# Optimization experiments

Measured on AMD Instinct MI355X. Metric: run time of the kernel, lower is better.

## Reference

```python
import jax, jax.numpy as jnp
import numpy as np

N_IN = 512
N_OUT = 256
K = 3
GRID_SIZE = N_OUT - K + 1  # 254
X_LO, X_HI = -1.0, 1.0
BATCH = 1024
LN_EPS = 1e-5


def make_grid():
    # grid_values: (n_in, grid_size + 2k + 1), identical rows as in the torch module
    step = (X_HI - X_LO) / GRID_SIZE
    g = jnp.linspace(X_LO - step * K, X_HI + step * K, GRID_SIZE + 2 * K + 1, dtype=jnp.float32)
    return jnp.broadcast_to(g, (N_IN, g.shape[0]))


def setup_inputs() -> dict:
    key = jax.random.key(0)
    k1, k2, k3 = jax.random.split(key, 3)
    x = jax.random.normal(k1, (BATCH, N_IN), dtype=jnp.float32)
    # kaiming-uniform-like scale for the linear weights
    weights = jax.random.normal(k2, (N_OUT, N_IN), dtype=jnp.float32) * (1.0 / np.sqrt(N_IN))
    spline_weights = jax.random.normal(k3, (N_OUT, N_IN, GRID_SIZE + K), dtype=jnp.float32) * (
        1.0 / np.sqrt(N_IN * (GRID_SIZE + K))
    )
    prelu_a = jnp.full((1,), 0.25, dtype=jnp.float32)  # PReLU default init
    return {"x": x, "weights": weights, "spline_weights": spline_weights, "prelu_a": prelu_a}


def reference(x, weights, spline_weights, prelu_a):
    g = make_grid()  # (n_in, P) with P = GRID_SIZE + 2K + 1
    # base branch: tanh(x) @ W^T
    b_out = jnp.tanh(x) @ weights.T  # (B, n_out)

    # Cox-de Boor recursion for B-spline bases
    xe = x[:, :, None]  # (B, n_in, 1)
    bases = ((xe >= g[:, :-1]) & (xe < g[:, 1:])).astype(x.dtype)  # (B, n_in, P-1)
    for k in range(1, K + 1):
        left = g[:, : -(k + 1)]
        right = g[:, k:-1]
        delta = jnp.where(right == left, jnp.ones_like(right), right - left)
        bases = (xe - left) / delta * bases[:, :, :-1] + (
            (g[:, k + 1 :] - xe) / (g[:, k + 1 :] - g[:, 1:-k])
        ) * bases[:, :, 1:]
    # bases: (B, n_in, GRID_SIZE + K)

    # flattened linear == einsum over (n_in, grid) axes
    spline_out = jnp.einsum("big,oig->bo", bases, spline_weights)  # (B, n_out)

    y = b_out + spline_out
    # LayerNorm without affine params
    mu = jnp.mean(y, axis=-1, keepdims=True)
    var = jnp.var(y, axis=-1, keepdims=True)
    yn = (y - mu) / jnp.sqrt(var + LN_EPS)
    # PReLU (single shared slope)
    return jnp.where(yn >= 0, yn, prelu_a[0] * yn)
```

## Files before the change

### kernel.cpp

```cpp
#include <hip/hip_runtime.h>
#include <hip/hip_fp16.h>
#include <math.h>

#define N_IN   512
#define N_OUT  256
#define NCOEF  257
#define BATCH  1024
#define LN_EPS 1e-5f
#define G0F (-1.0f - 3.0f * (2.0f / 254.0f))

#define ROWQ 20
#define NQ   129
#define SLABW (NQ * ROWQ)

#define SLOT(q_, oo_) ((q_) * ROWQ + (((((oo_) >> 2) ^ ((q_) & 3))) << 2) + ((oo_) & 3))

#define QP(v_, C_) ((unsigned)__builtin_amdgcn_mov_dpp((int)(v_), (C_), 0xf, 0xf, true))

static __device__ __forceinline__ unsigned pk_bf16x2(float a, float b) {
    unsigned ua = ((__float_as_uint(a) + 0x8000u) >> 16) & 0xffffu;
    unsigned ub = (__float_as_uint(b) + 0x8000u) & 0xffff0000u;
    return ua | ub;
}

static __device__ __forceinline__ float dot2bf(unsigned w, unsigned s, float c) {
    float d;
    asm("v_dot2_f32_bf16 %0, %1, %2, %3" : "=v"(d) : "v"(w), "v"(s), "v"(c));
    return d;
}

static __device__ __forceinline__ uint4 spline_pack(float xv) {
    const float e2 = __expf(2.f * xv);
    const float tx = 1.f - 2.f / (e2 + 1.f);
    const float u  = (xv - G0F) * 127.f;
    const bool has = (u >= 0.f) && (u < 260.f);
    const float uf = has ? u : 0.f;
    int m = (int)uf;
    if (m > 259) m = 259;
    const float tt = uf - (float)m;
    const float t2 = tt * tt, t3 = t2 * tt;
    const float omt = 1.f - tt;
    float a0 = omt * omt * omt * (1.f / 6.f);
    float a1 = (3.f * t3 - 6.f * t2 + 4.f) * (1.f / 6.f);
    float a2 = (-3.f * t3 + 3.f * t2 + 3.f * tt + 1.f) * (1.f / 6.f);
    float a3 = t3 * (1.f / 6.f);
    if (!has) { a0 = a1 = a2 = a3 = 0.f; }
    const int pb  = m - 3;
    const int pbc = pb < 0 ? 0 : (pb > 253 ? 253 : pb);
    const int d   = pbc - pb;
    if (d >= 1)  { a0 = a1; a1 = a2; a2 = a3; a3 = 0.f; }
    if (d >= 2)  { a0 = a1; a1 = a2; a2 = a3; a3 = 0.f; }
    if (d >= 3)  { a0 = a1; a1 = a2; a2 = a3; a3 = 0.f; }
    if (d <= -1) { a3 = a2; a2 = a1; a1 = a0; a0 = 0.f; }
    if (d <= -2) { a3 = a2; a2 = a1; a1 = a0; a0 = 0.f; }
    if (d <= -3) { a3 = a2; a2 = a1; a1 = a0; a0 = 0.f; }
    uint4 r;
    if (pbc & 1) {
        r.x = pk_bf16x2(0.f, a0);
        r.y = pk_bf16x2(a1, a2);
        r.z = pk_bf16x2(a3, 0.f);
    } else {
        r.x = pk_bf16x2(a0, a1);
        r.y = pk_bf16x2(a2, a3);
        r.z = 0u;
    }
    r.w = (unsigned)(pbc & ~1) |
          ((unsigned)__half_as_ushort(__float2half(tx)) << 16);
    return r;
}

__global__ __launch_bounds__(512, 4) void kan_main(
    const float* __restrict__ x, const float* __restrict__ W,
    const float* __restrict__ sw, float* __restrict__ part)
{
    const int bid = blockIdx.x;
    const int bc = bid & 1;
    const int oc = (bid >> 1) & 15;
    const int ig = bid >> 5;
    const int o0 = oc * 16, i0 = ig * 32, b0 = bc * 512;
    const int t = threadIdx.x;

    __shared__ __align__(16) unsigned slab[2][2][SLABW];
    __shared__ float Wl[2][2][16];

    const int wv = t >> 6, bl = (t >> 2) & 15, og = t & 3;
    const int soo = t & 15;
    const int sgc = t >> 4;

    const float* swrow = sw + ((size_t)(o0 + soo) * N_IN + i0) * NCOEF;
    const float* xp  = x + (size_t)(b0 + wv * 64 + og * 16 + bl) * N_IN + i0;
    const float* wgp = W + (size_t)(o0 + (t & 15)) * N_IN + i0 + (t >> 4);

    float4 A0, B0, A1, B1;
    float t0 = 0.f, t1 = 0.f, Wc = 0.f;
    float2 xc, xn, x2;

#define GLOAD(p) do {                                             \
        const float* _r0 = swrow + (size_t)(2 * (p)) * NCOEF;     \
        const float* _r1 = _r0 + NCOEF;                           \
        A0 = *(const float4*)&_r0[sgc * 4];                       \
        B0 = *(const float4*)&_r0[sgc * 4 + 128];                 \
        A1 = *(const float4*)&_r1[sgc * 4];                       \
        B1 = *(const float4*)&_r1[sgc * 4 + 128];                 \
        if (sgc == 31) { t0 = _r0[256]; t1 = _r1[256]; }          \
    } while (0)

#define STAGE(wb) do {                                            \
        unsigned* _s0 = &slab[wb][0][0];                          \
        unsigned* _s1 = &slab[wb][1][0];                          \
        const int _qa = 2 * sgc;                                  \
        _s0[SLOT(_qa,      soo)] = pk_bf16x2(A0.x, A0.y);         \
        _s0[SLOT(_qa + 1,  soo)] = pk_bf16x2(A0.z, A0.w);         \
        _s0[SLOT(_qa + 64, soo)] = pk_bf16x2(B0.x, B0.y);         \
        _s0[SLOT(_qa + 65, soo)] = pk_bf16x2(B0.z, B0.w);         \
        _s1[SLOT(_qa,      soo)] = pk_bf16x2(A1.x, A1.y);         \
        _s1[SLOT(_qa + 1,  soo)] = pk_bf16x2(A1.z, A1.w);         \
        _s1[SLOT(_qa + 64, soo)] = pk_bf16x2(B1.x, B1.y);         \
        _s1[SLOT(_qa + 65, soo)] = pk_bf16x2(B1.z, B1.w);         \
        if (sgc == 31) {                                          \
            _s0[SLOT(128, soo)] = pk_bf16x2(t0, 0.f);             \
            _s1[SLOT(128, soo)] = pk_bf16x2(t1, 0.f);             \
        }                                                         \
    } while (0)

#define DO_BP(bp_, CTRL_) do {                                                \
        uint4 ub;                                                             \
        ub.x = QP(u.x, CTRL_); ub.y = QP(u.y, CTRL_);                         \
        ub.z = QP(u.z, CTRL_); ub.w = QP(u.w, CTRL_);                         \
        const float tx =                                                      \
            __half2float(__ushort_as_half((unsigned short)(ub.w >> 16)));     \
        float4 a = acc[bp_];                                                  \
        a.x = fmaf(tx, Wv.x, a.x);                                            \
        a.y = fmaf(tx, Wv.y, a.y);                                            \
        a.z = fmaf(tx, Wv.z, a.z);                                            \
        a.w = fmaf(tx, Wv.w, a.w);                                            \
        if (ub.x | ub.y | ub.z) {                                             \
            const int q0 = (int)(ub.w & 0xffffu) >> 1;                        \
            _Pragma("unroll")                                                 \
            for (int j = 0; j < 3; ++j) {                                     \
                const int q = q0 + j;                                         \
                const unsigned wj = (j == 0) ? ub.x : (j == 1) ? ub.y : ub.z; \
                const uint4 s4 =                                              \
                    *(const uint4*)&sl[q * ROWQ + ((og ^ (q & 3)) << 2)];     \
                a.x = dot2bf(wj, s4.x, a.x);                                  \
                a.y = dot2bf(wj, s4.y, a.y);                                  \
                a.z = dot2bf(wj, s4.z, a.z);                                  \
                a.w = dot2bf(wj, s4.w, a.w);                                  \
            }                                                                 \
        }                                                                     \
        acc[bp_] = a;                                                         \
    } while (0)

    float4 acc[4];
#pragma unroll
    for (int bp = 0; bp < 4; ++bp) acc[bp] = make_float4(0.f, 0.f, 0.f, 0.f);

    GLOAD(0);
    xc = *(const float2*)&xp[0];
    if (t < 32) Wc = wgp[0];
    STAGE(0);
    if (t < 32) Wl[0][t >> 4][t & 15] = Wc;
    GLOAD(1);
    xn = *(const float2*)&xp[2];
    if (t < 32) Wc = wgp[2];
    x2 = xn;
    __syncthreads();

    int buf = 0;
    for (int n = 0; n < 16; ++n) {
        if (n + 1 < 16) {
            STAGE(buf ^ 1);
            if (t < 32) Wl[buf ^ 1][t >> 4][t & 15] = Wc;
            if (n + 2 < 16) {
                GLOAD(n + 2);
                x2 = *(const float2*)&xp[2 * (n + 2)];
                if (t < 32) Wc = wgp[2 * (n + 2)];
            }
        }

#pragma unroll
        for (int sub = 0; sub < 2; ++sub) {
            const uint4 u = spline_pack(sub == 0 ? xc.x : xc.y);
            const float4 Wv = *(const float4*)&Wl[buf][sub][og << 2];
            const unsigned* sl = &slab[buf][sub][0];
            DO_BP(0, 0x00);
            DO_BP(1, 0x55);
            DO_BP(2, 0xAA);
            DO_BP(3, 0xFF);
        }

        __syncthreads();
        buf ^= 1;
        xc = xn;
        xn = x2;
    }

    float* dst = part + ((size_t)ig * BATCH + b0 + wv * 64 + bl) * N_OUT
               + o0 + (og << 2);
#pragma unroll
    for (int bp = 0; bp < 4; ++bp)
        *reinterpret_cast<float4*>(&dst[(size_t)bp * 16 * N_OUT]) = acc[bp];
#undef GLOAD
#undef STAGE
#undef DO_BP
}

__global__ __launch_bounds__(256) void kan_ln(
    const float* __restrict__ part, const float* __restrict__ prelu_a,
    float* __restrict__ out)
{
    const int b = blockIdx.x;
    const int t = threadIdx.x;

    float sv = 0.f;
#pragma unroll
    for (int k = 0; k < 16; ++k)
        sv += part[((size_t)k * BATCH + b) * N_OUT + t];

    float v1 = sv, v2 = sv * sv;
#pragma unroll
    for (int d = 1; d < 64; d <<= 1) {
        v1 += __shfl_xor(v1, d);
        v2 += __shfl_xor(v2, d);
    }
    __shared__ float r1[4], r2[4];
    if ((t & 63) == 0) { r1[t >> 6] = v1; r2[t >> 6] = v2; }
    __syncthreads();
    const float tot1 = r1[0] + r1[1] + r1[2] + r1[3];
    const float tot2 = r2[0] + r2[1] + r2[2] + r2[3];

    const float mu  = tot1 * (1.f / N_OUT);
    const float var = tot2 * (1.f / N_OUT) - mu * mu;
    const float inv = rsqrtf(var + LN_EPS);
    const float yn  = (sv - mu) * inv;
    const float a   = prelu_a[0];
    out[(size_t)b * N_OUT + t] = (yn >= 0.f) ? yn : a * yn;
}

extern "C" void kernel_launch(void* const* d_in, const int* in_sizes, int n_in,
                              void* d_out, int out_size, void* d_ws, size_t ws_size,
                              hipStream_t stream)
{
    const float* x  = (const float*)d_in[0];
    const float* W  = (const float*)d_in[1];
    const float* sw = (const float*)d_in[2];
    const float* pa = (const float*)d_in[3];
    float* out  = (float*)d_out;
    float* part = (float*)d_ws;

    kan_main<<<dim3(512), 512, 0, stream>>>(x, W, sw, part);
    kan_ln  <<<dim3(1024), 256, 0, stream>>>(part, pa, out);
}
```

Baseline: 106.6 us.

## Split batch into quarters, single-buffer LDS slab, raise occupancy to six blocks

Doubles the grid so each block covers 256 batch rows instead of 512, halving the accumulators per thread. The LDS slab drops from double to single buffering, with two barriers per iteration. Spline packing for the next step is hoisted between compute phases, and launch bounds ask for six blocks per CU. The aim is more resident waves to hide latency, at the cost of reloading each spline-weight slab twice as often and adding an extra barrier per iteration.

```diff
diff --git a/kernel.cpp b/kernel.cpp
--- a/kernel.cpp
+++ b/kernel.cpp
@@ -69,31 +69,30 @@
     return r;
 }
 
-__global__ __launch_bounds__(512, 4) void kan_main(
+__global__ __launch_bounds__(512, 6) void kan_main(
     const float* __restrict__ x, const float* __restrict__ W,
     const float* __restrict__ sw, float* __restrict__ part)
 {
     const int bid = blockIdx.x;
-    const int bc = bid & 1;
-    const int oc = (bid >> 1) & 15;
-    const int ig = bid >> 5;
-    const int o0 = oc * 16, i0 = ig * 32, b0 = bc * 512;
+    const int bc = bid & 3;
+    const int oc = (bid >> 2) & 15;
+    const int ig = bid >> 6;
+    const int o0 = oc * 16, i0 = ig * 32, b0 = bc * 256;
     const int t = threadIdx.x;
 
-    __shared__ __align__(16) unsigned slab[2][2][SLABW];
-    __shared__ float Wl[2][2][16];
+    __shared__ __align__(16) unsigned slab[2][SLABW];
+    __shared__ float Wl[2][16];
 
     const int wv = t >> 6, bl = (t >> 2) & 15, og = t & 3;
     const int soo = t & 15;
     const int sgc = t >> 4;
 
     const float* swrow = sw + ((size_t)(o0 + soo) * N_IN + i0) * NCOEF;
-    const float* xp  = x + (size_t)(b0 + wv * 64 + og * 16 + bl) * N_IN + i0;
+    const float* xp  = x + (size_t)(b0 + wv * 32 + (og & 1) * 16 + bl) * N_IN + i0;
     const float* wgp = W + (size_t)(o0 + (t & 15)) * N_IN + i0 + (t >> 4);
 
     float4 A0, B0, A1, B1;
     float t0 = 0.f, t1 = 0.f, Wc = 0.f;
-    float2 xc, xn, x2;
 
 #define GLOAD(p) do {                                             \
         const float* _r0 = swrow + (size_t)(2 * (p)) * NCOEF;     \
@@ -105,9 +104,9 @@
         if (sgc == 31) { t0 = _r0[256]; t1 = _r1[256]; }          \
     } while (0)
 
-#define STAGE(wb) do {                                            \
-        unsigned* _s0 = &slab[wb][0][0];                          \
-        unsigned* _s1 = &slab[wb][1][0];                          \
+#define STAGE() do {                                              \
+        unsigned* _s0 = &slab[0][0];                              \
+        unsigned* _s1 = &slab[1][0];                              \
         const int _qa = 2 * sgc;                                  \
         _s0[SLOT(_qa,      soo)] = pk_bf16x2(A0.x, A0.y);         \
         _s0[SLOT(_qa + 1,  soo)] = pk_bf16x2(A0.z, A0.w);         \
@@ -123,10 +122,10 @@
         }                                                         \
     } while (0)
 
-#define DO_BP(bp_, CTRL_) do {                                                \
+#define DO_BP(bp_, CTRL_, upk_, sub_) do {                                    \
         uint4 ub;                                                             \
-        ub.x = QP(u.x, CTRL_); ub.y = QP(u.y, CTRL_);                         \
-        ub.z = QP(u.z, CTRL_); ub.w = QP(u.w, CTRL_);                         \
+        ub.x = QP((upk_).x, CTRL_); ub.y = QP((upk_).y, CTRL_);               \
+        ub.z = QP((upk_).z, CTRL_); ub.w = QP((upk_).w, CTRL_);               \
         const float tx =                                                      \
             __half2float(__ushort_as_half((unsigned short)(ub.w >> 16)));     \
         float4 a = acc[bp_];                                                  \
@@ -136,6 +135,7 @@
         a.w = fmaf(tx, Wv.w, a.w);                                            \
         if (ub.x | ub.y | ub.z) {                                             \
             const int q0 = (int)(ub.w & 0xffffu) >> 1;                        \
+            const unsigned* sl = &slab[sub_][0];                              \
             _Pragma("unroll")                                                 \
             for (int j = 0; j < 3; ++j) {                                     \
                 const int q = q0 + j;                                         \
@@ -151,55 +151,58 @@
         acc[bp_] = a;                                                         \
     } while (0)
 
-    float4 acc[4];
-#pragma unroll
-    for (int bp = 0; bp < 4; ++bp) acc[bp] = make_float4(0.f, 0.f, 0.f, 0.f);
+    float4 acc[2];
+    acc[0] = make_float4(0.f, 0.f, 0.f, 0.f);
+    acc[1] = make_float4(0.f, 0.f, 0.f, 0.f);
 
     GLOAD(0);
-    xc = *(const float2*)&xp[0];
+    float2 xc = *(const float2*)&xp[0];
     if (t < 32) Wc = wgp[0];
-    STAGE(0);
-    if (t < 32) Wl[0][t >> 4][t & 15] = Wc;
+    uint4 pk0 = spline_pack(xc.x);
+    uint4 pk1 = spline_pack(xc.y);
+    STAGE();
+    if (t < 32) Wl[t >> 4][t & 15] = Wc;
     GLOAD(1);
-    xn = *(const float2*)&xp[2];
+    float2 xn = *(const float2*)&xp[2];
     if (t < 32) Wc = wgp[2];
-    x2 = xn;
+    float2 xf = xn;
     __syncthreads();
 
-    int buf = 0;
     for (int n = 0; n < 16; ++n) {
+        {
+            const float4 Wv = *(const float4*)&Wl[0][og << 2];
+            DO_BP(0, 0x00, pk0, 0);
+            DO_BP(1, 0x55, pk0, 0);
+        }
+        const uint4 npk0 = spline_pack(xn.x);
+        {
+            const float4 Wv = *(const float4*)&Wl[1][og << 2];
+            DO_BP(0, 0x00, pk1, 1);
+            DO_BP(1, 0x55, pk1, 1);
+        }
+        const uint4 npk1 = spline_pack(xn.y);
+
+        __syncthreads();
+
         if (n + 1 < 16) {
-            STAGE(buf ^ 1);
-            if (t < 32) Wl[buf ^ 1][t >> 4][t & 15] = Wc;
+            STAGE();
+            if (t < 32) Wl[t >> 4][t & 15] = Wc;
             if (n + 2 < 16) {
                 GLOAD(n + 2);
-                x2 = *(const float2*)&xp[2 * (n + 2)];
+                xf = *(const float2*)&xp[2 * (n + 2)];
                 if (t < 32) Wc = wgp[2 * (n + 2)];
             }
+            __syncthreads();
         }
 
-#pragma unroll
-        for (int sub = 0; sub < 2; ++sub) {
-            const uint4 u = spline_pack(sub == 0 ? xc.x : xc.y);
-            const float4 Wv = *(const float4*)&Wl[buf][sub][og << 2];
-            const unsigned* sl = &slab[buf][sub][0];
-            DO_BP(0, 0x00);
-            DO_BP(1, 0x55);
-            DO_BP(2, 0xAA);
-            DO_BP(3, 0xFF);
-        }
-
-        __syncthreads();
-        buf ^= 1;
-        xc = xn;
-        xn = x2;
+        pk0 = npk0; pk1 = npk1;
+        xn = xf;
     }
 
-    float* dst = part + ((size_t)ig * BATCH + b0 + wv * 64 + bl) * N_OUT
+    float* dst = part + ((size_t)ig * BATCH + b0 + wv * 32 + bl) * N_OUT
                + o0 + (og << 2);
-#pragma unroll
-    for (int bp = 0; bp < 4; ++bp)
-        *reinterpret_cast<float4*>(&dst[(size_t)bp * 16 * N_OUT]) = acc[bp];
+    *reinterpret_cast<float4*>(&dst[0]) = acc[0];
+    *reinterpret_cast<float4*>(&dst[(size_t)16 * N_OUT]) = acc[1];
 #undef GLOAD
 #undef STAGE
 #undef DO_BP
@@ -248,6 +251,6 @@
     float* out  = (float*)d_out;
     float* part = (float*)d_ws;
 
-    kan_main<<<dim3(512), 512, 0, stream>>>(x, W, sw, part);
+    kan_main<<<dim3(1024), 512, 0, stream>>>(x, W, sw, part);
     kan_ln  <<<dim3(1024), 256, 0, stream>>>(part, pa, out);
 }
```

Result: slower. 140.0 us (+31.3%).
